# Optimization experiments

Measured on AMD Instinct MI355X. Metric: run time of the kernel, lower is better.

## Reference

```python
import jax, jax.numpy as jnp
import numpy as np

HIDDEN = 4096
LATENT = 32768


def setup_inputs() -> dict:
    key = jax.random.key(0)
    k1, k2, k3, k4, k5 = jax.random.split(key, 5)
    x = jax.random.normal(k1, (2, 2048, HIDDEN), dtype=jnp.float32)
    # learned params (loaded from checkpoint in the original; random here)
    pre_bias = jax.random.normal(k2, (HIDDEN,), dtype=jnp.float32) * 0.02
    latent_bias = jax.random.normal(k3, (LATENT,), dtype=jnp.float32) * 0.02
    # nn.Linear weights: encoder.weight [latent, hidden], decoder.weight [hidden, latent]
    enc_w = jax.random.normal(k4, (LATENT, HIDDEN), dtype=jnp.float32) / np.sqrt(HIDDEN)
    dec_w = jax.random.normal(k5, (HIDDEN, LATENT), dtype=jnp.float32) / np.sqrt(LATENT)
    return {"x": x, "pre_bias": pre_bias, "latent_bias": latent_bias,
            "enc_w": enc_w, "dec_w": dec_w, "k": 64}


def reference(x, pre_bias, latent_bias, enc_w, dec_w, k):
    B, S, H = x.shape
    L = enc_w.shape[0]
    # pre_acts = encoder(x - pre_bias) + latent_bias
    pre_acts = jnp.einsum('bsh,lh->bsl', x - pre_bias, enc_w) + latent_bias
    # TopK sparsification: keep top-k values per token, zero elsewhere
    flat = pre_acts.reshape(B * S, L)
    vals, idx = jax.lax.top_k(flat, k)                       # [N,k]
    rows = jnp.arange(B * S)[:, None]                        # [N,1]
    latents = jnp.zeros_like(flat).at[rows, idx].set(vals).reshape(B, S, L)
    # x_hat = decoder(latents) + pre_bias
    x_hat = jnp.einsum('bsl,hl->bsh', latents, dec_w) + pre_bias
    return latents, x_hat
```

## Files before the change

kernel.cpp:

```cpp
#include <hip/hip_runtime.h>
#include <hip/hip_fp16.h>

typedef unsigned short u16;
typedef unsigned int u32;
using f32x4 = __attribute__((ext_vector_type(4))) float;
using bf16x8 = __attribute__((ext_vector_type(8))) short;

#define M_TOK 4096
#define HID   4096
#define LAT   32768
#define TOPK  64

#define BM 256
#define BN 256
#define BK 64
#define NT (HID / BK)
#define LCAP 2048
#define CAND_T0 2.0f
#define WBAND 0.0625f

__device__ __forceinline__ u16 f2bf(float f) {
  u32 u = __builtin_bit_cast(u32, f);
  u32 r = 0x7fffu + ((u >> 16) & 1u);
  return (u16)((u + r) >> 16);
}

__global__ __launch_bounds__(256) void k_xs(const float* __restrict__ x,
                                            const float* __restrict__ pb,
                                            u16* __restrict__ xs) {
  size_t i = ((size_t)blockIdx.x * 256 + threadIdx.x) * 4;
  if (i >= (size_t)M_TOK * HID) return;
  float4 xv = *(const float4*)(x + i);
  float4 bv = *(const float4*)(pb + (i & (HID - 1)));
  ushort4 o;
  o.x = f2bf(xv.x - bv.x); o.y = f2bf(xv.y - bv.y);
  o.z = f2bf(xv.z - bv.z); o.w = f2bf(xv.w - bv.w);
  *(ushort4*)(xs + i) = o;
}

__global__ __launch_bounds__(256) void k_conv(const float* __restrict__ src,
                                              u16* __restrict__ dst, size_t n4) {
  size_t i = (size_t)blockIdx.x * 256 + threadIdx.x;
  size_t stride = (size_t)gridDim.x * 256;
  for (; i < n4; i += stride) {
    float4 v = ((const float4*)src)[i];
    ushort4 o;
    o.x = f2bf(v.x); o.y = f2bf(v.y); o.z = f2bf(v.z); o.w = f2bf(v.w);
    ((ushort4*)dst)[i] = o;
  }
}

__global__ __launch_bounds__(512, 2) void k_gemm(const u16* __restrict__ A,
                                                 const u16* __restrict__ B,
                                                 const float* __restrict__ lbias,
                                                 float2* __restrict__ lists,
                                                 int* __restrict__ cnt) {
  __shared__ __align__(16) u16 Asm[2][2][128][64];
  __shared__ __align__(16) u16 Bsm[2][2][128][64];
  const int tid = threadIdx.x;
  const int lane = tid & 63;
  const int wave = tid >> 6;
  const int wm = wave >> 2;
  const int wn = wave & 3;

  const int bid = blockIdx.x;
  const int wg = (bid & 7) * 256 + (bid >> 3);
  const int bm = (wg & 15) * BM;
  const int bn = (wg >> 4) * BN;

  const int spr = tid >> 3, ss = tid & 7;
  const int slcol = (ss ^ (spr & 7)) << 3;
  const int spr2 = spr + 64;
  const int slcol2 = (ss ^ (spr2 & 7)) << 3;

  auto stageA2 = [&](int t) {
    int b = t & 1;
#pragma unroll
    for (int h = 0; h < 2; ++h) {
      __builtin_amdgcn_global_load_lds(
          (const __attribute__((address_space(1))) void*)(
              A + (size_t)(bm + h * 128 + spr) * HID + t * BK + slcol),
          (__attribute__((address_space(3))) void*)(&Asm[b][h][spr][ss << 3]), 16, 0, 0);
      __builtin_amdgcn_global_load_lds(
          (const __attribute__((address_space(1))) void*)(
              A + (size_t)(bm + h * 128 + spr2) * HID + t * BK + slcol2),
          (__attribute__((address_space(3))) void*)(&Asm[b][h][spr2][ss << 3]), 16, 0, 0);
    }
  };
  auto stageB2 = [&](int t) {
    int b = t & 1;
#pragma unroll
    for (int h = 0; h < 2; ++h) {
      __builtin_amdgcn_global_load_lds(
          (const __attribute__((address_space(1))) void*)(
              B + (size_t)(bn + h * 128 + spr) * HID + t * BK + slcol),
          (__attribute__((address_space(3))) void*)(&Bsm[b][h][spr][ss << 3]), 16, 0, 0);
      __builtin_amdgcn_global_load_lds(
          (const __attribute__((address_space(1))) void*)(
              B + (size_t)(bn + h * 128 + spr2) * HID + t * BK + slcol2),
          (__attribute__((address_space(3))) void*)(&Bsm[b][h][spr2][ss << 3]), 16, 0, 0);
    }
  };

  auto readA = [&](int b, int m, int ks) -> bf16x8 {
    int pr = m * 16 + (lane & 15);
    int pe = (ks * 32 + ((lane >> 4) << 3)) ^ ((pr & 7) << 3);
    return *(const bf16x8*)(&Asm[b][wm][pr][pe]);
  };
  auto readB = [&](int b, int n, int ks) -> bf16x8 {
    int pr = (wn & 1) * 64 + n * 16 + (lane & 15);
    int pe = (ks * 32 + ((lane >> 4) << 3)) ^ ((pr & 7) << 3);
    return *(const bf16x8*)(&Bsm[b][wn >> 1][pr][pe]);
  };

  f32x4 acc[8][4] = {};
  bf16x8 a[4][2], b[4][2];

#define BAR() __builtin_amdgcn_s_barrier()
#define PRIO1() __builtin_amdgcn_s_setprio(1)
#define PRIO0() __builtin_amdgcn_s_setprio(0)
#define VMCNT8() asm volatile("s_waitcnt vmcnt(8)" ::: "memory")
#define VMCNT0() asm volatile("s_waitcnt vmcnt(0)" ::: "memory")

  stageB2(0); stageA2(0); stageB2(1); stageA2(1);
  VMCNT8();
  BAR();

#pragma unroll 1
  for (int i = 0; i < NT / 2; ++i) {
    const int t0 = 2 * i, t1 = 2 * i + 1;
#pragma unroll
    for (int half = 0; half < 2; ++half) {
      const int bf = half;
      const int tn = half ? t1 + 2 : t0 + 2;
#pragma unroll
      for (int m = 0; m < 4; ++m)
#pragma unroll
        for (int ks = 0; ks < 2; ++ks) a[m][ks] = readA(bf, m, ks);
#pragma unroll
      for (int n = 0; n < 2; ++n)
#pragma unroll
        for (int ks = 0; ks < 2; ++ks) b[n][ks] = readB(bf, n, ks);
      BAR(); PRIO1();
#pragma unroll
      for (int ks = 0; ks < 2; ++ks)
#pragma unroll
        for (int m = 0; m < 4; ++m)
#pragma unroll
          for (int n = 0; n < 2; ++n)
            acc[m][n] = __builtin_amdgcn_mfma_f32_16x16x32_bf16(a[m][ks], b[n][ks], acc[m][n], 0, 0, 0);
      PRIO0(); BAR();
#pragma unroll
      for (int n = 2; n < 4; ++n)
#pragma unroll
        for (int ks = 0; ks < 2; ++ks) b[n][ks] = readB(bf, n, ks);
      BAR(); PRIO1();
#pragma unroll
      for (int ks = 0; ks < 2; ++ks)
#pragma unroll
        for (int m = 0; m < 4; ++m)
#pragma unroll
          for (int n = 2; n < 4; ++n)
            acc[m][n] = __builtin_amdgcn_mfma_f32_16x16x32_bf16(a[m][ks], b[n][ks], acc[m][n], 0, 0, 0);
      PRIO0(); BAR();
#pragma unroll
      for (int m = 0; m < 4; ++m)
#pragma unroll
        for (int ks = 0; ks < 2; ++ks) a[m][ks] = readA(bf, m + 4, ks);
      if (tn < NT) stageB2(tn);
      BAR(); PRIO1();
#pragma unroll
      for (int ks = 0; ks < 2; ++ks)
#pragma unroll
        for (int m = 0; m < 4; ++m)
#pragma unroll
          for (int n = 2; n < 4; ++n)
            acc[m + 4][n] = __builtin_amdgcn_mfma_f32_16x16x32_bf16(a[m][ks], b[n][ks], acc[m + 4][n], 0, 0, 0);
      PRIO0(); BAR();
      if (tn < NT) {
        stageA2(tn);
        VMCNT8();
      } else {
        VMCNT0();
      }
      BAR(); PRIO1();
#pragma unroll
      for (int ks = 0; ks < 2; ++ks)
#pragma unroll
        for (int m = 0; m < 4; ++m)
#pragma unroll
          for (int n = 0; n < 2; ++n)
            acc[m + 4][n] = __builtin_amdgcn_mfma_f32_16x16x32_bf16(a[m][ks], b[n][ks], acc[m + 4][n], 0, 0, 0);
      PRIO0(); BAR();
    }
  }

#pragma unroll
  for (int n = 0; n < 4; ++n) {
    int col = bn + wn * 64 + n * 16 + (lane & 15);
    float lb = lbias[col];
#pragma unroll
    for (int m = 0; m < 8; ++m) {
      int row = bm + wm * 128 + m * 16 + ((lane >> 4) << 2);
#pragma unroll
      for (int j = 0; j < 4; ++j) {
        float v = acc[m][n][j] + lb;
        if (v >= CAND_T0) {
          int p = atomicAdd(&cnt[row + j], 1);
          if (p < LCAP)
            lists[(size_t)(row + j) * LCAP + p] =
                make_float2(v, __builtin_bit_cast(float, col));
        }
      }
    }
  }
#undef BAR
#undef PRIO1
#undef PRIO0
#undef VMCNT8
#undef VMCNT0
}

__global__ __launch_bounds__(256) void k_topk(
    const float2* __restrict__ lists, const int* __restrict__ cnt,
    const float* __restrict__ x,
    const float* __restrict__ pb,
    const float* __restrict__ enc_w,
    const float* __restrict__ lbias,
    int* __restrict__ oidx, float* __restrict__ oval) {
  const int row = blockIdx.x;
  const int tid = threadIdx.x;
  const int lane = tid & 63, wave = tid >> 6;

  __shared__ int cnum, innum, selnum;
  __shared__ float s_m;
  __shared__ int lidx[LCAP];
  __shared__ float laf[LCAP];
  __shared__ int cidx[352];
  __shared__ double cref[352];
  __shared__ int fidx[64];
  __shared__ float fval[64];

  const int n = min(cnt[row], LCAP);
  if (tid == 0) { s_m = -1e30f; cnum = 0; innum = 0; selnum = 0; }
  for (int j = tid; j < n; j += 256) {
    float2 e = lists[(size_t)row * LCAP + j];
    laf[j] = e.x;
    lidx[j] = __builtin_bit_cast(int, e.y);
  }
  __syncthreads();

  for (int j = tid; j < n; j += 256) {
    float aj = laf[j]; int ij = lidx[j];
    int rank = 0;
    for (int i2 = 0; i2 < n; ++i2) {
      float ai = laf[i2];
      rank += (ai > aj) || (ai == aj && lidx[i2] < ij);
    }
    if (rank == 63) s_m = aj;
  }
  __syncthreads();
  float mf = s_m;

  for (int j = tid; j < n; j += 256) {
    float aa = laf[j];
    if (aa > mf + WBAND) {
      int p = atomicAdd(&innum, 1);
      if (p < 64) { fidx[p] = lidx[j]; fval[p] = aa; }
    } else if (aa >= mf - WBAND) {
      int p = atomicAdd(&cnum, 1);
      if (p < 352) cidx[p] = lidx[j];
    }
  }
  __syncthreads();
  int nin = min(innum, 64);
  int nu = min(cnum, 352);

  const float* xrow = x + (size_t)row * HID;
  for (int cc = wave; cc < nu; cc += 4) {
    const float* wrow = enc_w + (size_t)cidx[cc] * HID;
    double s = 0.0;
    for (int i = lane * 4; i < HID; i += 256) {
      float4 wv = *(const float4*)(wrow + i);
      float4 xv = *(const float4*)(xrow + i);
      float4 bv = *(const float4*)(pb + i);
      s += ((double)xv.x - (double)bv.x) * (double)wv.x;
      s += ((double)xv.y - (double)bv.y) * (double)wv.y;
      s += ((double)xv.z - (double)bv.z) * (double)wv.z;
      s += ((double)xv.w - (double)bv.w) * (double)wv.w;
    }
#pragma unroll
    for (int off = 32; off > 0; off >>= 1) s += __shfl_down(s, off);
    if (lane == 0) cref[cc] = s + (double)lbias[cidx[cc]];
  }
  __syncthreads();

  int need = 64 - nin;
  for (int j = tid; j < nu; j += 256) {
    double rj = cref[j]; int ij = cidx[j];
    int rank = 0;
    for (int i2 = 0; i2 < nu; ++i2) {
      double ri = cref[i2];
      rank += (ri > rj) || (ri == rj && cidx[i2] < ij);
    }
    if (rank < need) {
      int p = atomicAdd(&selnum, 1);
      if (nin + p < 64) { fidx[nin + p] = ij; fval[nin + p] = (float)rj; }
    }
  }
  __syncthreads();

  if (tid < 64) {
    int my = fidx[tid]; float v = fval[tid];
    int rank = 0;
#pragma unroll
    for (int i2 = 0; i2 < 64; ++i2) rank += (fidx[i2] < my);
    oidx[row * 64 + rank] = my;
    oval[row * 64 + rank] = v;
  }
}

__global__ __launch_bounds__(256) void k_trans(const float* __restrict__ dw,
                                               u16* __restrict__ dt) {
  __shared__ float tile[64][65];
  int l0 = blockIdx.x * 64;
  int h0 = blockIdx.y * 64;
  int tx = threadIdx.x & 15;
  int ty = threadIdx.x >> 4;
#pragma unroll
  for (int i = 0; i < 4; ++i) {
    int r = ty + i * 16;
    float4 v = *(const float4*)(dw + (size_t)(h0 + r) * LAT + l0 + tx * 4);
    tile[r][tx * 4 + 0] = v.x; tile[r][tx * 4 + 1] = v.y;
    tile[r][tx * 4 + 2] = v.z; tile[r][tx * 4 + 3] = v.w;
  }
  __syncthreads();
#pragma unroll
  for (int i = 0; i < 4; ++i) {
    int r = ty + i * 16;
    ushort4 o;
    o.x = f2bf(tile[tx * 4 + 0][r]);
    o.y = f2bf(tile[tx * 4 + 1][r]);
    o.z = f2bf(tile[tx * 4 + 2][r]);
    o.w = f2bf(tile[tx * 4 + 3][r]);
    *(ushort4*)(dt + (size_t)(l0 + r) * HID + h0 + tx * 4) = o;
  }
}

__global__ __launch_bounds__(256) void k_decode(
    const int* __restrict__ oidx, const float* __restrict__ oval,
    const u16* __restrict__ dt, const float* __restrict__ pb,
    float* __restrict__ xh) {
  const int n = blockIdx.x, tid = threadIdx.x;
  __shared__ int sidx[64];
  __shared__ float sval[64];
  if (tid < 64) { sidx[tid] = oidx[n * 64 + tid]; sval[tid] = oval[n * 64 + tid]; }
  __syncthreads();
  const int h0 = tid * 16;
  float acc[16];
#pragma unroll
  for (int q = 0; q < 4; ++q) {
    float4 b = *(const float4*)(pb + h0 + q * 4);
    acc[q * 4 + 0] = b.x; acc[q * 4 + 1] = b.y;
    acc[q * 4 + 2] = b.z; acc[q * 4 + 3] = b.w;
  }
  for (int j = 0; j < 64; ++j) {
    float v = sval[j];
    const uint4* w = (const uint4*)(dt + (size_t)sidx[j] * HID + h0);
    uint4 p0 = w[0], p1 = w[1];
    u32 u[8] = {p0.x, p0.y, p0.z, p0.w, p1.x, p1.y, p1.z, p1.w};
#pragma unroll
    for (int q = 0; q < 8; ++q) {
      float lo = __builtin_bit_cast(float, u[q] << 16);
      float hi = __builtin_bit_cast(float, u[q] & 0xffff0000u);
      acc[q * 2 + 0] = fmaf(v, lo, acc[q * 2 + 0]);
      acc[q * 2 + 1] = fmaf(v, hi, acc[q * 2 + 1]);
    }
  }
#pragma unroll
  for (int q = 0; q < 4; ++q) {
    float4 o;
    o.x = acc[q * 4 + 0]; o.y = acc[q * 4 + 1];
    o.z = acc[q * 4 + 2]; o.w = acc[q * 4 + 3];
    *(float4*)(xh + (size_t)n * HID + h0 + q * 4) = o;
  }
}

__global__ __launch_bounds__(256) void k_lat(const int* __restrict__ oidx,
                                             const float* __restrict__ oval,
                                             float* __restrict__ lat) {
  const int n = blockIdx.x, tid = threadIdx.x;
  __shared__ int sidx[64];
  __shared__ float sval[64];
  if (tid < 64) { sidx[tid] = oidx[n * 64 + tid]; sval[tid] = oval[n * 64 + tid]; }
  float* row = lat + (size_t)n * LAT;
  float4 z = {0.f, 0.f, 0.f, 0.f};
  for (int q = tid; q < LAT / 4; q += 256) *(float4*)(row + q * 4) = z;
  __syncthreads();
  if (tid < 64) row[sidx[tid]] = sval[tid];
}

extern "C" void kernel_launch(void* const* d_in, const int* in_sizes, int n_in,
                              void* d_out, int out_size, void* d_ws, size_t ws_size,
                              hipStream_t stream) {
  const float* x = (const float*)d_in[0];
  const float* pre_bias = (const float*)d_in[1];
  const float* latent_bias = (const float*)d_in[2];
  const float* enc_w = (const float*)d_in[3];
  const float* dec_w = (const float*)d_in[4];

  float* latents = (float*)d_out;
  float* xhat = latents + (size_t)M_TOK * LAT;

  u16* xs = (u16*)xhat;
  u16* encb = (u16*)latents;
  float2* lists = (float2*)((char*)d_out + (size_t)M_TOK * LAT * 2);
  u16* decT = (u16*)latents;
  int* cnt = (int*)d_ws;
  int* oidx = (int*)((char*)d_ws + M_TOK * 4);
  float* oval = (float*)((char*)d_ws + M_TOK * 4 + (size_t)M_TOK * TOPK * 4);

  hipMemsetAsync(cnt, 0, M_TOK * 4, stream);
  k_xs<<<(M_TOK * HID / 4 + 255) / 256, 256, 0, stream>>>(x, pre_bias, xs);
  k_conv<<<4096, 256, 0, stream>>>(enc_w, encb, (size_t)LAT * HID / 4);
  k_gemm<<<(LAT / BN) * (M_TOK / BM), 512, 0, stream>>>(xs, encb, latent_bias, lists, cnt);
  k_topk<<<M_TOK, 256, 0, stream>>>(lists, cnt, x, pre_bias, enc_w, latent_bias, oidx, oval);
  k_trans<<<dim3(LAT / 64, HID / 64), 256, 0, stream>>>(dec_w, decT);
  k_decode<<<M_TOK, 256, 0, stream>>>(oidx, oval, decT, pre_bias, xhat);
  k_lat<<<M_TOK, 256, 0, stream>>>(oidx, oval, latents);
}
```

Before: 2.531 ms.

## Shrink encoder GEMM tile to 256x128x32 with simple double-buffered loop

Replaces the 256x256x64 encoder GEMM tile and its hand-scheduled barrier/priority pipeline with a 256x128 tile and K step of 32. The new version uses a plain double-buffered loop with one __syncthreads per K step and a repacked, swizzled LDS layout. Launch bounds move from 2 to 4 blocks per CU, aiming for more occupancy through smaller LDS and register footprints. The trade-off is lower arithmetic intensity per tile, more global traffic, more barriers per FLOP, and loss of the fine-grained MFMA/load interleaving.

```diff
diff --git a/kernel.cpp b/kernel.cpp
--- a/kernel.cpp
+++ b/kernel.cpp
@@ -12,8 +12,8 @@
 #define TOPK  64
 
 #define BM 256
-#define BN 256
-#define BK 64
+#define BN 128
+#define BK 32
 #define NT (HID / BK)
 #define LCAP 2048
 #define CAND_T0 2.0f
@@ -50,149 +50,89 @@
   }
 }
 
-__global__ __launch_bounds__(512, 2) void k_gemm(const u16* __restrict__ A,
+__global__ __launch_bounds__(512, 4) void k_gemm(const u16* __restrict__ A,
                                                  const u16* __restrict__ B,
                                                  const float* __restrict__ lbias,
                                                  float2* __restrict__ lists,
                                                  int* __restrict__ cnt) {
-  __shared__ __align__(16) u16 Asm[2][2][128][64];
-  __shared__ __align__(16) u16 Bsm[2][2][128][64];
+  __shared__ __align__(16) u16 Asm[2][128][64];
+  __shared__ __align__(16) u16 Bsm[2][64][64];
   const int tid = threadIdx.x;
   const int lane = tid & 63;
   const int wave = tid >> 6;
-  const int wm = wave >> 2;
-  const int wn = wave & 3;
+  const int wm = wave >> 1;
+  const int wn = wave & 1;
 
   const int bid = blockIdx.x;
-  const int wg = (bid & 7) * 256 + (bid >> 3);
+  const int wg = (bid & 7) * 512 + (bid >> 3);
   const int bm = (wg & 15) * BM;
   const int bn = (wg >> 4) * BN;
 
-  const int spr = tid >> 3, ss = tid & 7;
-  const int slcol = (ss ^ (spr & 7)) << 3;
-  const int spr2 = spr + 64;
-  const int slcol2 = (ss ^ (spr2 & 7)) << 3;
-
-  auto stageA2 = [&](int t) {
+  const int sp = tid >> 3, sslot = tid & 7;
+  const int ss0 = sslot ^ (sp & 7);
+  const int sr = sp * 2 + (ss0 >> 2);
+  const int sc = (ss0 & 3) << 3;
+  const int sp2 = sp + 64;
+  const int ss02 = sslot ^ (sp2 & 7);
+  const int sr2 = sp2 * 2 + (ss02 >> 2);
+  const int sc2 = (ss02 & 3) << 3;
+
+  auto stage = [&](int t) {
     int b = t & 1;
-#pragma unroll
-    for (int h = 0; h < 2; ++h) {
+    __builtin_amdgcn_global_load_lds(
+        (const __attribute__((address_space(1))) void*)(
+            A + (size_t)(bm + sr) * HID + t * BK + sc),
+        (__attribute__((address_space(3))) void*)(&Asm[b][sp][sslot << 3]), 16, 0, 0);
+    __builtin_amdgcn_global_load_lds(
+        (const __attribute__((address_space(1))) void*)(
+            A + (size_t)(bm + sr2) * HID + t * BK + sc2),
+        (__attribute__((address_space(3))) void*)(&Asm[b][sp2][sslot << 3]), 16, 0, 0);
+    if (sp < 64)
       __builtin_amdgcn_global_load_lds(
           (const __attribute__((address_space(1))) void*)(
-              A + (size_t)(bm + h * 128 + spr) * HID + t * BK + slcol),
-          (__attribute__((address_space(3))) void*)(&Asm[b][h][spr][ss << 3]), 16, 0, 0);
+              B + (size_t)(bn + sr) * HID + t * BK + sc),
+          (__attribute__((address_space(3))) void*)(&Bsm[b][sp][sslot << 3]), 16, 0, 0);
+    else
       __builtin_amdgcn_global_load_lds(
           (const __attribute__((address_space(1))) void*)(
-              A + (size_t)(bm + h * 128 + spr2) * HID + t * BK + slcol2),
-          (__attribute__((address_space(3))) void*)(&Asm[b][h][spr2][ss << 3]), 16, 0, 0);
-    }
+              B + (size_t)(bn + sr - 128) * HID + t * BK + sc),
+          (__attribute__((address_space(3))) void*)(&Bsm[b][sp - 64][sslot << 3]), 16, 0, 0);
   };
-  auto stageB2 = [&](int t) {
-    int b = t & 1;
-#pragma unroll
-    for (int h = 0; h < 2; ++h) {
-      __builtin_amdgcn_global_load_lds(
-          (const __attribute__((address_space(1))) void*)(
-              B + (size_t)(bn + h * 128 + spr) * HID + t * BK + slcol),
-          (__attribute__((address_space(3))) void*)(&Bsm[b][h][spr][ss << 3]), 16, 0, 0);
-      __builtin_amdgcn_global_load_lds(
-          (const __attribute__((address_space(1))) void*)(
-              B + (size_t)(bn + h * 128 + spr2) * HID + t * BK + slcol2),
-          (__attribute__((address_space(3))) void*)(&Bsm[b][h][spr2][ss << 3]), 16, 0, 0);
-    }
+
+  const int chunk = lane >> 4;
+  auto readA = [&](int b, int m) -> bf16x8 {
+    int r = wm * 64 + m * 16 + (lane & 15);
+    int p = r >> 1;
+    int s = (((r & 1) << 2) + chunk) ^ (p & 7);
+    return *(const bf16x8*)(&Asm[b][p][s << 3]);
   };
-
-  auto readA = [&](int b, int m, int ks) -> bf16x8 {
-    int pr = m * 16 + (lane & 15);
-    int pe = (ks * 32 + ((lane >> 4) << 3)) ^ ((pr & 7) << 3);
-    return *(const bf16x8*)(&Asm[b][wm][pr][pe]);
+  auto readB = [&](int b, int n) -> bf16x8 {
+    int r = wn * 64 + n * 16 + (lane & 15);
+    int p = r >> 1;
+    int s = (((r & 1) << 2) + chunk) ^ (p & 7);
+    return *(const bf16x8*)(&Bsm[b][p][s << 3]);
   };
-  auto readB = [&](int b, int n, int ks) -> bf16x8 {
-    int pr = (wn & 1) * 64 + n * 16 + (lane & 15);
-    int pe = (ks * 32 + ((lane >> 4) << 3)) ^ ((pr & 7) << 3);
-    return *(const bf16x8*)(&Bsm[b][wn >> 1][pr][pe]);
-  };
-
-  f32x4 acc[8][4] = {};
-  bf16x8 a[4][2], b[4][2];
-
-#define BAR() __builtin_amdgcn_s_barrier()
-#define PRIO1() __builtin_amdgcn_s_setprio(1)
-#define PRIO0() __builtin_amdgcn_s_setprio(0)
-#define VMCNT8() asm volatile("s_waitcnt vmcnt(8)" ::: "memory")
-#define VMCNT0() asm volatile("s_waitcnt vmcnt(0)" ::: "memory")
-
-  stageB2(0); stageA2(0); stageB2(1); stageA2(1);
-  VMCNT8();
-  BAR();
+
+  f32x4 acc[4][4] = {};
+
+  stage(0);
+  __syncthreads();
 
 #pragma unroll 1
-  for (int i = 0; i < NT / 2; ++i) {
-    const int t0 = 2 * i, t1 = 2 * i + 1;
-#pragma unroll
-    for (int half = 0; half < 2; ++half) {
-      const int bf = half;
-      const int tn = half ? t1 + 2 : t0 + 2;
-#pragma unroll
-      for (int m = 0; m < 4; ++m)
-#pragma unroll
-        for (int ks = 0; ks < 2; ++ks) a[m][ks] = readA(bf, m, ks);
-#pragma unroll
-      for (int n = 0; n < 2; ++n)
-#pragma unroll
-        for (int ks = 0; ks < 2; ++ks) b[n][ks] = readB(bf, n, ks);
-      BAR(); PRIO1();
-#pragma unroll
-      for (int ks = 0; ks < 2; ++ks)
-#pragma unroll
-        for (int m = 0; m < 4; ++m)
-#pragma unroll
-          for (int n = 0; n < 2; ++n)
-            acc[m][n] = __builtin_amdgcn_mfma_f32_16x16x32_bf16(a[m][ks], b[n][ks], acc[m][n], 0, 0, 0);
-      PRIO0(); BAR();
-#pragma unroll
-      for (int n = 2; n < 4; ++n)
-#pragma unroll
-        for (int ks = 0; ks < 2; ++ks) b[n][ks] = readB(bf, n, ks);
-      BAR(); PRIO1();
-#pragma unroll
-      for (int ks = 0; ks < 2; ++ks)
-#pragma unroll
-        for (int m = 0; m < 4; ++m)
-#pragma unroll
-          for (int n = 2; n < 4; ++n)
-            acc[m][n] = __builtin_amdgcn_mfma_f32_16x16x32_bf16(a[m][ks], b[n][ks], acc[m][n], 0, 0, 0);
-      PRIO0(); BAR();
-#pragma unroll
-      for (int m = 0; m < 4; ++m)
-#pragma unroll
-        for (int ks = 0; ks < 2; ++ks) a[m][ks] = readA(bf, m + 4, ks);
-      if (tn < NT) stageB2(tn);
-      BAR(); PRIO1();
-#pragma unroll
-      for (int ks = 0; ks < 2; ++ks)
-#pragma unroll
-        for (int m = 0; m < 4; ++m)
-#pragma unroll
-          for (int n = 2; n < 4; ++n)
-            acc[m + 4][n] = __builtin_amdgcn_mfma_f32_16x16x32_bf16(a[m][ks], b[n][ks], acc[m + 4][n], 0, 0, 0);
-      PRIO0(); BAR();
-      if (tn < NT) {
-        stageA2(tn);
-        VMCNT8();
-      } else {
-        VMCNT0();
-      }
-      BAR(); PRIO1();
-#pragma unroll
-      for (int ks = 0; ks < 2; ++ks)
-#pragma unroll
-        for (int m = 0; m < 4; ++m)
-#pragma unroll
-          for (int n = 0; n < 2; ++n)
-            acc[m + 4][n] = __builtin_amdgcn_mfma_f32_16x16x32_bf16(a[m][ks], b[n][ks], acc[m + 4][n], 0, 0, 0);
-      PRIO0(); BAR();
-    }
+  for (int t = 0; t < NT; ++t) {
+    const int b = t & 1;
+    if (t + 1 < NT) stage(t + 1);
+    bf16x8 a[4], bb[4];
+#pragma unroll
+    for (int m = 0; m < 4; ++m) a[m] = readA(b, m);
+#pragma unroll
+    for (int n = 0; n < 4; ++n) bb[n] = readB(b, n);
+#pragma unroll
+    for (int m = 0; m < 4; ++m)
+#pragma unroll
+      for (int n = 0; n < 4; ++n)
+        acc[m][n] = __builtin_amdgcn_mfma_f32_16x16x32_bf16(a[m], bb[n], acc[m][n], 0, 0, 0);
+    __syncthreads();
   }
 
 #pragma unroll
@@ -200,8 +140,8 @@
     int col = bn + wn * 64 + n * 16 + (lane & 15);
     float lb = lbias[col];
 #pragma unroll
-    for (int m = 0; m < 8; ++m) {
-      int row = bm + wm * 128 + m * 16 + ((lane >> 4) << 2);
+    for (int m = 0; m < 4; ++m) {
+      int row = bm + wm * 64 + m * 16 + ((lane >> 4) << 2);
 #pragma unroll
       for (int j = 0; j < 4; ++j) {
         float v = acc[m][n][j] + lb;
@@ -214,11 +154,6 @@
       }
     }
   }
-#undef BAR
-#undef PRIO1
-#undef PRIO0
-#undef VMCNT8
-#undef VMCNT0
 }
 
 __global__ __launch_bounds__(256) void k_topk(
@@ -423,7 +358,7 @@
   hipMemsetAsync(cnt, 0, M_TOK * 4, stream);
   k_xs<<<(M_TOK * HID / 4 + 255) / 256, 256, 0, stream>>>(x, pre_bias, xs);
   k_conv<<<4096, 256, 0, stream>>>(enc_w, encb, (size_t)LAT * HID / 4);
-  k_gemm<<<(LAT / BN) * (M_TOK / BM), 512, 0, stream>>>(xs, encb, latent_bias, lists, cnt);
+  k_gemm<<<(M_TOK / BM) * (LAT / BN), 512, 0, stream>>>(xs, encb, latent_bias, lists, cnt);
   k_topk<<<M_TOK, 256, 0, stream>>>(lists, cnt, x, pre_bias, enc_w, latent_bias, oidx, oval);
   k_trans<<<dim3(LAT / 64, HID / 64), 256, 0, stream>>>(dec_w, decT);
   k_decode<<<M_TOK, 256, 0, stream>>>(oidx, oval, decT, pre_bias, xhat);
```

Result: slower. 2.682 ms (+5.9%).
